# Performance work log

Measured on AMD Instinct MI355X. Metric: run time of the kernel, lower is better.

Reference implementation:

```python
import jax, jax.numpy as jnp
import numpy as np

B, S, D = 4, 2048, 256
H = 8
KD = D  # keras MHA key_dim = input_shape[-1] -> per-head dim equals D
EPS = 1e-5


def layer_norm(x, gamma, beta):
    mu = jnp.mean(x, axis=-1, keepdims=True)
    var = jnp.var(x, axis=-1, keepdims=True)
    return (x - mu) * jax.lax.rsqrt(var + EPS) * gamma + beta


def setup_inputs() -> dict:
    key = jax.random.key(0)
    ks = jax.random.split(key, 12)
    scale = 1.0 / np.sqrt(D)
    inp = {
        "input_query": jax.random.normal(ks[0], (B, S, D), jnp.float32),
        "key": jax.random.normal(ks[1], (B, S, D), jnp.float32),
        "value": jax.random.normal(ks[2], (B, S, D), jnp.float32),
        # LayerNorm params (3 separate norms)
        "gq": jnp.ones((D,), jnp.float32), "bq_ln": jnp.zeros((D,), jnp.float32),
        "gk": jnp.ones((D,), jnp.float32), "bk_ln": jnp.zeros((D,), jnp.float32),
        "gv": jnp.ones((D,), jnp.float32), "bv_ln": jnp.zeros((D,), jnp.float32),
        # MHA projection weights: [D, H, KD] for q/k/v, [H, KD, D] for output
        "Wq": jax.random.normal(ks[3], (D, H, KD), jnp.float32) * scale,
        "bq": jnp.zeros((H, KD), jnp.float32),
        "Wk": jax.random.normal(ks[4], (D, H, KD), jnp.float32) * scale,
        "bk": jnp.zeros((H, KD), jnp.float32),
        "Wv": jax.random.normal(ks[5], (D, H, KD), jnp.float32) * scale,
        "bv": jnp.zeros((H, KD), jnp.float32),
        "Wo": jax.random.normal(ks[6], (H, KD, D), jnp.float32) * scale,
        "bo": jnp.zeros((D,), jnp.float32),
    }
    return inp


def reference(input_query, key, value, gq, bq_ln, gk, bk_ln, gv, bv_ln,
              Wq, bq, Wk, bk, Wv, bv, Wo, bo):
    # pre-LN on each stream
    q_in = layer_norm(input_query, gq, bq_ln)
    k_in = layer_norm(key, gk, bk_ln)
    v_in = layer_norm(value, gv, bv_ln)

    # projections -> [B, S, H, KD]
    q = jnp.einsum('bsd,dhk->bshk', q_in, Wq) + bq
    k = jnp.einsum('bsd,dhk->bshk', k_in, Wk) + bk
    v = jnp.einsum('bsd,dhk->bshk', v_in, Wv) + bv

    # scaled dot-product attention (keras scales query by 1/sqrt(key_dim))
    q = q * (1.0 / np.sqrt(KD)).astype(np.float32)
    scores = jnp.einsum('bqhk,bshk->bhqs', q, k)  # [B, H, Sq, Sk]
    probs = jax.nn.softmax(scores, axis=-1)
    # dropout = 0.0 (inference)
    attn = jnp.einsum('bhqs,bshk->bqhk', probs, v)
    out = jnp.einsum('bqhk,hkd->bqd', attn, Wo) + bo

    return input_query + out
```

## Files before the change

### kernel.cpp

```cpp
#include <hip/hip_runtime.h>

using bf16x8 = __attribute__((ext_vector_type(8))) __bf16;
using f32x4  = __attribute__((ext_vector_type(4))) float;
using f32x16 = __attribute__((ext_vector_type(16))) float;
using uint2v = __attribute__((ext_vector_type(2))) unsigned;
typedef unsigned short u16;
typedef const __attribute__((address_space(1))) void* gas_p;
typedef __attribute__((address_space(3))) void* las_p;

#define LOG2E 1.4426950408889634f

__device__ __forceinline__ u16 f2bf(float f) {
  union { float f; unsigned u; } v; v.f = f;
  unsigned r = v.u + 0x7fffu + ((v.u >> 16) & 1u);
  return (u16)(r >> 16);
}

__device__ __forceinline__ unsigned pkbf(float a, float b) {
  unsigned r;
  asm("v_cvt_pk_bf16_f32 %0, %1, %2" : "=v"(r) : "v"(a), "v"(b));
  return r;
}

__device__ __forceinline__ float exp2v(float x) {
  float r;
  asm("v_exp_f32 %0, %1" : "=v"(r) : "v"(x));
  return r;
}

__device__ __forceinline__ unsigned pk_fp8x4(float a, float b, float c, float d) {
  int w = __builtin_amdgcn_cvt_pk_fp8_f32(a, b, 0, false);
  w = __builtin_amdgcn_cvt_pk_fp8_f32(c, d, w, true);
  return (unsigned)w;
}

__device__ __forceinline__ uint2v swap32(unsigned a, unsigned b) {
  return __builtin_amdgcn_permlane32_swap(a, b, false, false);
}

__device__ __forceinline__ void gload16(const void* g, void* l) {
  __builtin_amdgcn_global_load_lds((gas_p)g, (las_p)l, 16, 0, 0);
}

#define MFMA(a, b, c)   __builtin_amdgcn_mfma_f32_16x16x32_bf16((a), (b), (c), 0, 0, 0)
#define MFMA32(a, b, c) __builtin_amdgcn_mfma_f32_32x32x16_bf16((a), (b), (c), 0, 0, 0)
#define MFMA8(a, b, c)  __builtin_amdgcn_mfma_f32_32x32x16_fp8_fp8((a), (b), (c), 0, 0, 0)

__global__ __launch_bounds__(256) void transpose_conv(
    const float* __restrict__ Wq, const float* __restrict__ Wk,
    const float* __restrict__ Wv, const float* __restrict__ Wo,
    u16* __restrict__ wqt, u16* __restrict__ wkt,
    u16* __restrict__ wvt, u16* __restrict__ wot)
{
  int z = blockIdx.y;
  const float* src = (z == 0) ? Wq : (z == 1) ? Wk : (z == 2) ? Wv : Wo;
  u16* dst = (z == 0) ? wqt : (z == 1) ? wkt : (z == 2) ? wvt : wot;
  int C = (z < 3) ? 2048 : 256;
  int R = (z < 3) ? 256 : 2048;
  int TC = C >> 5;
  int tc = blockIdx.x % TC, tr = blockIdx.x / TC;
  __shared__ float tile[32][33];
  int j = threadIdx.x & 31, i0 = threadIdx.x >> 5;
#pragma unroll
  for (int p = 0; p < 4; p++)
    tile[i0 + p * 8][j] = src[(tr * 32 + i0 + p * 8) * C + tc * 32 + j];
  __syncthreads();
#pragma unroll
  for (int p = 0; p < 4; p++)
    dst[(tc * 32 + i0 + p * 8) * R + tr * 32 + j] = f2bf(tile[j][i0 + p * 8]);
}

__global__ __launch_bounds__(256) void ln3_kernel(
    const float* __restrict__ xq, const float* __restrict__ xk, const float* __restrict__ xv,
    const float* __restrict__ gq, const float* __restrict__ bq,
    const float* __restrict__ gk, const float* __restrict__ bk,
    const float* __restrict__ gv, const float* __restrict__ bv,
    u16* __restrict__ oq, u16* __restrict__ ok, u16* __restrict__ ov)
{
  int z = blockIdx.y;
  const float* x = (z == 0) ? xq : (z == 1) ? xk : xv;
  const float* g = (z == 0) ? gq : (z == 1) ? gk : gv;
  const float* be = (z == 0) ? bq : (z == 1) ? bk : bv;
  u16* o = (z == 0) ? oq : (z == 1) ? ok : ov;
  int w = threadIdx.x >> 6, l = threadIdx.x & 63;
  int row = blockIdx.x * 4 + w;
  float4 x4 = *(const float4*)(x + row * 256 + l * 4);
  float s = x4.x + x4.y + x4.z + x4.w;
  float sq = x4.x * x4.x + x4.y * x4.y + x4.z * x4.z + x4.w * x4.w;
#pragma unroll
  for (int mm = 1; mm < 64; mm <<= 1) { s += __shfl_xor(s, mm); sq += __shfl_xor(sq, mm); }
  float mu = s * (1.f / 256.f);
  float var = sq * (1.f / 256.f) - mu * mu;
  float rs = rsqrtf(var + 1e-5f);
  float4 g4 = *(const float4*)(g + l * 4);
  float4 b4 = *(const float4*)(be + l * 4);
  ushort4 o4;
  o4.x = f2bf((x4.x - mu) * rs * g4.x + b4.x);
  o4.y = f2bf((x4.y - mu) * rs * g4.y + b4.y);
  o4.z = f2bf((x4.z - mu) * rs * g4.z + b4.z);
  o4.w = f2bf((x4.w - mu) * rs * g4.w + b4.w);
  *(ushort4*)(o + row * 256 + l * 4) = o4;
}

__global__ __launch_bounds__(256) void proj_gemm_qk(
    const u16* __restrict__ qn, const u16* __restrict__ kn,
    const u16* __restrict__ wqt, const u16* __restrict__ wkt,
    const float* __restrict__ bq, const float* __restrict__ bk,
    u16* __restrict__ qo, u16* __restrict__ ko)
{
  __shared__ u16 As[128 * 64];
  __shared__ u16 Bs[128 * 64];
  int z = blockIdx.z;
  const u16* A  = z ? kn : qn;
  const u16* Bt = z ? wkt : wqt;
  const float* bias = z ? bk : bq;
  u16* Co = z ? ko : qo;
  float scale = z ? 1.0f : 0.0625f * LOG2E;

  int i0 = blockIdx.x * 128, n0 = blockIdx.y * 128;
  int tid = threadIdx.x, w = tid >> 6, l = tid & 63;
  int wr = w >> 1, wc = w & 1, l15 = l & 15, qv = l >> 4;

  f32x4 acc[4][4] = {};

  for (int k0 = 0; k0 < 256; k0 += 64) {
    __syncthreads();
#pragma unroll
    for (int j = 0; j < 4; j++) {
      int c = (w * 4 + j) * 64 + l;
      int row = c >> 3, co = (c & 7) * 8;
      gload16(A + (i0 + row) * 256 + k0 + co, (char*)As + (w * 4 + j) * 1024);
      gload16(Bt + (n0 + row) * 256 + k0 + co, (char*)Bs + (w * 4 + j) * 1024);
    }
    __syncthreads();
#pragma unroll
    for (int kk = 0; kk < 2; kk++) {
      bf16x8 a[4], bfr[4];
#pragma unroll
      for (int m = 0; m < 4; m++)
        a[m] = *(const bf16x8*)(As + (wr * 64 + m * 16 + l15) * 64 + kk * 32 + qv * 8);
#pragma unroll
      for (int n = 0; n < 4; n++)
        bfr[n] = *(const bf16x8*)(Bs + (wc * 64 + n * 16 + l15) * 64 + kk * 32 + qv * 8);
#pragma unroll
      for (int m = 0; m < 4; m++)
#pragma unroll
        for (int n = 0; n < 4; n++) acc[m][n] = MFMA(bfr[n], a[m], acc[m][n]);
    }
  }

#pragma unroll
  for (int m = 0; m < 4; m++) {
    int row = i0 + wr * 64 + m * 16 + l15;
    int bb = row >> 11, ss = row & 2047;
#pragma unroll
    for (int n = 0; n < 4; n++) {
      int col0 = n0 + wc * 64 + n * 16 + qv * 4;
      float4 bc4 = *(const float4*)(bias + col0);
      int hd = col0 >> 8, kd0 = col0 & 255;
      ushort4 o4;
      o4.x = f2bf((acc[m][n][0] + bc4.x) * scale);
      o4.y = f2bf((acc[m][n][1] + bc4.y) * scale);
      o4.z = f2bf((acc[m][n][2] + bc4.z) * scale);
      o4.w = f2bf((acc[m][n][3] + bc4.w) * scale);
      *(ushort4*)(Co + ((size_t)(bb * 8 + hd) * 2048 + ss) * 256 + kd0) = o4;
    }
  }
}

__global__ __launch_bounds__(256) void proj_gemm_v(
    const u16* __restrict__ vn, const u16* __restrict__ wvt,
    const float* __restrict__ bv, unsigned char* __restrict__ vo)
{
  __shared__ u16 As[128 * 64];
  __shared__ u16 Bs[128 * 64];
  int i0 = blockIdx.x * 128, n0 = blockIdx.y * 128;
  int tid = threadIdx.x, w = tid >> 6, l = tid & 63;
  int wr = w >> 1, wc = w & 1, l15 = l & 15, qv = l >> 4;

  f32x4 acc[4][4] = {};

  for (int k0 = 0; k0 < 256; k0 += 64) {
    __syncthreads();
#pragma unroll
    for (int j = 0; j < 4; j++) {
      int c = (w * 4 + j) * 64 + l;
      int row = c >> 3, co = (c & 7) * 8;
      gload16(vn + (i0 + row) * 256 + k0 + co, (char*)As + (w * 4 + j) * 1024);
      gload16(wvt + (n0 + row) * 256 + k0 + co, (char*)Bs + (w * 4 + j) * 1024);
    }
    __syncthreads();
#pragma unroll
    for (int kk = 0; kk < 2; kk++) {
      bf16x8 a[4], bfr[4];
#pragma unroll
      for (int m = 0; m < 4; m++)
        a[m] = *(const bf16x8*)(As + (wr * 64 + m * 16 + l15) * 64 + kk * 32 + qv * 8);
#pragma unroll
      for (int n = 0; n < 4; n++)
        bfr[n] = *(const bf16x8*)(Bs + (wc * 64 + n * 16 + l15) * 64 + kk * 32 + qv * 8);
#pragma unroll
      for (int m = 0; m < 4; m++)
#pragma unroll
        for (int n = 0; n < 4; n++) acc[m][n] = MFMA(a[m], bfr[n], acc[m][n]);
    }
  }

#pragma unroll
  for (int n = 0; n < 4; n++) {
    int col = n0 + wc * 64 + n * 16 + l15;
    float bc = bv[col];
    int hd = col >> 8, kd = col & 255;
#pragma unroll
    for (int m = 0; m < 4; m++) {
      int row0 = i0 + wr * 64 + m * 16 + qv * 4;
      int bb = row0 >> 11, ss = row0 & 2047;
      unsigned wv = pk_fp8x4(acc[m][n][0] + bc, acc[m][n][1] + bc,
                             acc[m][n][2] + bc, acc[m][n][3] + bc);
      int pos = (ss & ~63) | (((ss >> 3) & 3) << 4) | (((ss >> 5) & 1) << 3) | (ss & 7);
      *(unsigned*)(vo + ((size_t)(bb * 8 + hd) * 256 + kd) * 2048 + pos) = wv;
    }
  }
}

__global__ __launch_bounds__(512, 2) void flash_attn(
    const u16* __restrict__ q, const u16* __restrict__ k,
    const unsigned char* __restrict__ vt, u16* __restrict__ o)
{
  __shared__ char lds[98304];
  int f = blockIdx.x;
  int qt = f >> 5;
  int bh = (f & 7) | (((f >> 3) & 3) << 3);
  int b = bh >> 3, hh = bh & 7;
  int tid = threadIdx.x, w = tid >> 6, l = tid & 63;
  int l31 = l & 31, h = l >> 5;

  const u16* Q = q + (size_t)(bh * 2048 + qt * 256 + w * 32) * 256;
  const u16* K = k + (size_t)bh * 2048 * 256;
  const unsigned char* V = vt + (size_t)bh * 256 * 2048;

  bf16x8 qf[16];
#pragma unroll
  for (int dt = 0; dt < 16; dt++)
    qf[dt] = *(const bf16x8*)(Q + l31 * 256 + dt * 16 + h * 8);

  f32x16 oacc[8] = {};
  float m_ = -1e30f, lsum = 0.f;

  auto stage = [&](int t, char* base) {
#pragma unroll
    for (int j = 0; j < 4; j++) {
      int c = w * 4 + j;
      int off = c * 1024 + l * 16;
      int r = off >> 9, ps = l & 31;
      gload16(K + (size_t)(t * 64 + r) * 256 + ((ps ^ (r & 31)) << 3), base + off);
    }
#pragma unroll
    for (int j = 0; j < 2; j++) {
      int c = w * 2 + j;
      int off = c * 1024 + l * 16;
      int r = off >> 8, pg = (off >> 4) & 15;
      int g = pg ^ (r & 15);
      int d = r + 64 * (g >> 2), sc = g & 3;
      gload16(V + (size_t)d * 2048 + t * 64 + sc * 16, base + 32768 + off);
    }
  };

  stage(0, lds);
  __syncthreads();

  for (int t = 0; t < 32; t++) {
    char* cur = lds + (size_t)(t & 1) * 49152;
    char* nxt = lds + (size_t)((t + 1) & 1) * 49152;
    if (t + 1 < 32) stage(t + 1, nxt);

    f32x16 p0 = {}, p1 = {};
    __builtin_amdgcn_s_setprio(1);
#pragma unroll
    for (int dt = 0; dt < 16; dt++) {
      int sl = ((dt * 2 + h) ^ l31) << 4;
      bf16x8 kf0 = *(const bf16x8*)(cur + l31 * 512 + sl);
      bf16x8 kf1 = *(const bf16x8*)(cur + (32 + l31) * 512 + sl);
      p0 = MFMA32(kf0, qf[dt], p0);
      p1 = MFMA32(kf1, qf[dt], p1);
    }
    __builtin_amdgcn_s_setprio(0);

    float n0 = fmaxf(fmaxf(p0[0], p0[1]), fmaxf(p0[2], p0[3]));
    float n1 = fmaxf(fmaxf(p0[4], p0[5]), fmaxf(p0[6], p0[7]));
    float n2 = fmaxf(fmaxf(p0[8], p0[9]), fmaxf(p0[10], p0[11]));
    float n3 = fmaxf(fmaxf(p0[12], p0[13]), fmaxf(p0[14], p0[15]));
    float n4 = fmaxf(fmaxf(p1[0], p1[1]), fmaxf(p1[2], p1[3]));
    float n5 = fmaxf(fmaxf(p1[4], p1[5]), fmaxf(p1[6], p1[7]));
    float n6 = fmaxf(fmaxf(p1[8], p1[9]), fmaxf(p1[10], p1[11]));
    float n7 = fmaxf(fmaxf(p1[12], p1[13]), fmaxf(p1[14], p1[15]));
    float mt = fmaxf(fmaxf(fmaxf(n0, n1), fmaxf(n2, n3)),
                     fmaxf(fmaxf(n4, n5), fmaxf(n6, n7)));
    {
      uint2v mr = swap32(__builtin_bit_cast(unsigned, mt), __builtin_bit_cast(unsigned, mt));
      mt = fmaxf(__builtin_bit_cast(float, mr.x), __builtin_bit_cast(float, mr.y));
    }
    if (__any(mt > m_ + 7.0f)) {
      float mn = fmaxf(m_, mt);
      float fsc = exp2v(m_ - mn);
      lsum *= fsc;
#pragma unroll
      for (int dt = 0; dt < 8; dt++)
#pragma unroll
        for (int i = 0; i < 16; i++) oacc[dt][i] *= fsc;
      m_ = mn;
    }
#pragma unroll
    for (int i = 0; i < 16; i++) { p0[i] = exp2v(p0[i] - m_); lsum += p0[i]; }
#pragma unroll
    for (int i = 0; i < 16; i++) { p1[i] = exp2v(p1[i] - m_); lsum += p1[i]; }

    unsigned pwf0[4], pwf1[4];
#pragma unroll
    for (int j = 0; j < 4; j++) {
      pwf0[j] = pk_fp8x4(p0[4 * j], p0[4 * j + 1], p0[4 * j + 2], p0[4 * j + 3]);
      pwf1[j] = pk_fp8x4(p1[4 * j], p1[4 * j + 1], p1[4 * j + 2], p1[4 * j + 3]);
    }

#pragma unroll
    for (int k2 = 0; k2 < 2; k2++) {
      uint2v f0 = swap32(pwf0[k2 * 2], pwf0[k2 * 2 + 1]);
      uint2v f1 = swap32(pwf1[k2 * 2], pwf1[k2 * 2 + 1]);
      long long pA = (long long)(((unsigned long long)f0.y << 32) | f0.x);
      long long pB = (long long)(((unsigned long long)f1.y << 32) | f1.x);
      __builtin_amdgcn_s_setprio(1);
#pragma unroll
      for (int dt = 0; dt < 8; dt++) {
        int r = (dt & 1) * 32 + l31;
        int g = (dt >> 1) * 4 + k2 * 2 + h;
        const uint4 vv = *(const uint4*)(cur + 32768 + r * 256 + ((g ^ (r & 15)) << 4));
        long long vA = (long long)(((unsigned long long)vv.y << 32) | vv.x);
        long long vB = (long long)(((unsigned long long)vv.w << 32) | vv.z);
        oacc[dt] = MFMA8(vA, pA, oacc[dt]);
        oacc[dt] = MFMA8(vB, pB, oacc[dt]);
      }
      __builtin_amdgcn_s_setprio(0);
    }

    asm volatile("s_waitcnt vmcnt(0)" ::: "memory");
    __syncthreads();
  }

  __syncthreads();
  float lsc;
  {
    uint2v lr = swap32(__builtin_bit_cast(unsigned, lsum), __builtin_bit_cast(unsigned, lsum));
    lsc = __builtin_bit_cast(float, lr.x) + __builtin_bit_cast(float, lr.y);
  }
  float inv = 1.0f / lsc;
  char* wbase = (char*)lds + w * 8192;
  int qr15 = l31 & 15;
#pragma unroll
  for (int ph = 0; ph < 2; ph++) {
    if ((l31 >> 4) == ph) {
#pragma unroll
      for (int dt = 0; dt < 8; dt++) {
#pragma unroll
        for (int rg = 0; rg < 4; rg++) {
          uint2 uu;
          uu.x = pkbf(oacc[dt][rg * 4 + 0] * inv, oacc[dt][rg * 4 + 1] * inv);
          uu.y = pkbf(oacc[dt][rg * 4 + 2] * inv, oacc[dt][rg * 4 + 3] * inv);
          *(uint2*)(wbase + qr15 * 512 + ((dt * 64 + rg * 16) ^ (qr15 << 4)) + h * 8) = uu;
        }
      }
    }
    asm volatile("s_waitcnt lgkmcnt(0)" ::: "memory");
    __builtin_amdgcn_sched_barrier(0);
#pragma unroll
    for (int c = 0; c < 8; c++) {
      int qr = c * 2 + h;
      uint4 vv = *(const uint4*)(wbase + qr * 512 + ((l31 ^ qr) << 4));
      int s = qt * 256 + w * 32 + ph * 16 + qr;
      *(uint4*)((char*)o + (size_t)(b * 2048 + s) * 4096 + hh * 512 + l31 * 16) = vv;
    }
    asm volatile("s_waitcnt lgkmcnt(0)" ::: "memory");
  }
}

__global__ __launch_bounds__(256) void out_gemm(
    const u16* __restrict__ A, const u16* __restrict__ Bt,
    const float* __restrict__ bo, const float* __restrict__ resid,
    float* __restrict__ out)
{
  __shared__ u16 As[64 * 64];
  __shared__ u16 Bs[64 * 64];
  int i0 = blockIdx.x * 64, n0 = blockIdx.y * 64;
  int tid = threadIdx.x, w = tid >> 6, l = tid & 63, l15 = l & 15, qv = l >> 4;

  f32x4 acc[4] = {};

  for (int k0 = 0; k0 < 2048; k0 += 64) {
    __syncthreads();
#pragma unroll
    for (int j = 0; j < 2; j++) {
      int c = w * 2 + j;
      int off = c * 1024 + l * 16;
      int r = off >> 7, co = (off & 127) >> 1;
      gload16(A + (size_t)(i0 + r) * 2048 + k0 + co, (char*)As + off);
      gload16(Bt + (size_t)(n0 + r) * 2048 + k0 + co, (char*)Bs + off);
    }
    __syncthreads();
#pragma unroll
    for (int kk = 0; kk < 2; kk++) {
      bf16x8 a = *(const bf16x8*)(As + (w * 16 + l15) * 64 + kk * 32 + qv * 8);
      bf16x8 bfr[4];
#pragma unroll
      for (int n = 0; n < 4; n++)
        bfr[n] = *(const bf16x8*)(Bs + (n * 16 + l15) * 64 + kk * 32 + qv * 8);
#pragma unroll
      for (int n = 0; n < 4; n++) acc[n] = MFMA(bfr[n], a, acc[n]);
    }
  }

  int row = i0 + w * 16 + l15;
#pragma unroll
  for (int n = 0; n < 4; n++) {
    int col0 = n0 + n * 16 + qv * 4;
    float4 bc4 = *(const float4*)(bo + col0);
    float4 rs4 = *(const float4*)(resid + (size_t)row * 256 + col0);
    float4 o4;
    o4.x = acc[n][0] + bc4.x + rs4.x;
    o4.y = acc[n][1] + bc4.y + rs4.y;
    o4.z = acc[n][2] + bc4.z + rs4.z;
    o4.w = acc[n][3] + bc4.w + rs4.w;
    *(float4*)(out + (size_t)row * 256 + col0) = o4;
  }
}

extern "C" void kernel_launch(void* const* d_in, const int* in_sizes, int n_in,
                              void* d_out, int out_size, void* d_ws, size_t ws_size,
                              hipStream_t stream)
{
  const float* inq  = (const float*)d_in[0];
  const float* key  = (const float*)d_in[1];
  const float* val  = (const float*)d_in[2];
  const float* gq   = (const float*)d_in[3];
  const float* bqln = (const float*)d_in[4];
  const float* gk   = (const float*)d_in[5];
  const float* bkln = (const float*)d_in[6];
  const float* gv   = (const float*)d_in[7];
  const float* bvln = (const float*)d_in[8];
  const float* Wq   = (const float*)d_in[9];
  const float* bq   = (const float*)d_in[10];
  const float* Wk   = (const float*)d_in[11];
  const float* bk   = (const float*)d_in[12];
  const float* Wv   = (const float*)d_in[13];
  const float* bv   = (const float*)d_in[14];
  const float* Wo   = (const float*)d_in[15];
  const float* bo   = (const float*)d_in[16];

  char* ws = (char*)d_ws;
  const size_t MB = 1ull << 20;
  u16* wqt = (u16*)(ws + 0 * MB);
  u16* wkt = (u16*)(ws + 1 * MB);
  u16* wvt = (u16*)(ws + 2 * MB);
  u16* wot = (u16*)(ws + 3 * MB);
  u16* qn  = (u16*)(ws + 4 * MB);
  u16* kn  = (u16*)(ws + 8 * MB);
  u16* vn  = (u16*)(ws + 12 * MB);
  u16* qws = (u16*)(ws + 16 * MB);
  u16* kws = (u16*)(ws + 48 * MB);
  u16* attn = (u16*)(ws + 80 * MB);
  unsigned char* vtw = (unsigned char*)(ws + 112 * MB);

  transpose_conv<<<dim3(512, 4), 256, 0, stream>>>(Wq, Wk, Wv, Wo, wqt, wkt, wvt, wot);
  ln3_kernel<<<dim3(2048, 3), 256, 0, stream>>>(inq, key, val, gq, bqln, gk, bkln, gv, bvln,
                                                qn, kn, vn);
  proj_gemm_qk<<<dim3(64, 16, 2), 256, 0, stream>>>(qn, kn, wqt, wkt, bq, bk, qws, kws);
  proj_gemm_v<<<dim3(64, 16), 256, 0, stream>>>(vn, wvt, bv, vtw);
  flash_attn<<<256, 512, 0, stream>>>(qws, kws, vtw, attn);
  out_gemm<<<dim3(128, 4), 256, 0, stream>>>(attn, wot, bo, inq, (float*)d_out);
}
```

Baseline: 253.1 us.

## Shrink flash-attn blocks to 4 waves and split K/V staging pipeline

The attention kernel now launches 512 blocks of 256 threads, each covering 128 query rows instead of 256, and changes the block-to-(batch,head) mapping. K tiles stay double-buffered, but V is single-buffered and loaded at the start of each iteration. A partial vmcnt wait plus a barrier sits before the PV stage, so the V load overlaps the QK^T and softmax work. The aim is more blocks for load balance across CUs and a smaller LDS footprint. The cost is that each block reloads all of K and V, doubling K/V traffic, and each iteration has an extra barrier.

```diff
diff --git a/kernel.cpp b/kernel.cpp
--- a/kernel.cpp
+++ b/kernel.cpp
@@ -223,19 +223,20 @@
   }
 }
 
-__global__ __launch_bounds__(512, 2) void flash_attn(
+__global__ __launch_bounds__(256, 2) void flash_attn(
     const u16* __restrict__ q, const u16* __restrict__ k,
     const unsigned char* __restrict__ vt, u16* __restrict__ o)
 {
-  __shared__ char lds[98304];
+  __shared__ char lds[81920];
   int f = blockIdx.x;
-  int qt = f >> 5;
-  int bh = (f & 7) | (((f >> 3) & 3) << 3);
+  int idx = f >> 3;
+  int bh = (f & 7) * 4 + (idx & 3);
+  int qt = idx >> 2;
   int b = bh >> 3, hh = bh & 7;
   int tid = threadIdx.x, w = tid >> 6, l = tid & 63;
   int l31 = l & 31, h = l >> 5;
 
-  const u16* Q = q + (size_t)(bh * 2048 + qt * 256 + w * 32) * 256;
+  const u16* Q = q + (size_t)(bh * 2048 + qt * 128 + w * 32) * 256;
   const u16* K = k + (size_t)bh * 2048 * 256;
   const unsigned char* V = vt + (size_t)bh * 256 * 2048;
 
@@ -247,40 +248,45 @@
   f32x16 oacc[8] = {};
   float m_ = -1e30f, lsum = 0.f;
 
-  auto stage = [&](int t, char* base) {
-#pragma unroll
-    for (int j = 0; j < 4; j++) {
-      int c = w * 4 + j;
+  auto stageK = [&](int t, int slot) {
+    char* base = lds + (size_t)slot * 32768;
+#pragma unroll
+    for (int j = 0; j < 8; j++) {
+      int c = w * 8 + j;
       int off = c * 1024 + l * 16;
       int r = off >> 9, ps = l & 31;
       gload16(K + (size_t)(t * 64 + r) * 256 + ((ps ^ (r & 31)) << 3), base + off);
     }
-#pragma unroll
-    for (int j = 0; j < 2; j++) {
-      int c = w * 2 + j;
+  };
+  auto stageV = [&](int t) {
+    char* base = lds + 65536;
+#pragma unroll
+    for (int j = 0; j < 4; j++) {
+      int c = w * 4 + j;
       int off = c * 1024 + l * 16;
       int r = off >> 8, pg = (off >> 4) & 15;
       int g = pg ^ (r & 15);
       int d = r + 64 * (g >> 2), sc = g & 3;
-      gload16(V + (size_t)d * 2048 + t * 64 + sc * 16, base + 32768 + off);
+      gload16(V + (size_t)d * 2048 + t * 64 + sc * 16, base + off);
     }
   };
 
-  stage(0, lds);
+  stageK(0, 0);
+  asm volatile("s_waitcnt vmcnt(0)" ::: "memory");
   __syncthreads();
 
   for (int t = 0; t < 32; t++) {
-    char* cur = lds + (size_t)(t & 1) * 49152;
-    char* nxt = lds + (size_t)((t + 1) & 1) * 49152;
-    if (t + 1 < 32) stage(t + 1, nxt);
+    const char* kb = lds + (size_t)(t & 1) * 32768;
+    stageV(t);
+    if (t + 1 < 32) stageK(t + 1, (t + 1) & 1);
 
     f32x16 p0 = {}, p1 = {};
     __builtin_amdgcn_s_setprio(1);
 #pragma unroll
     for (int dt = 0; dt < 16; dt++) {
       int sl = ((dt * 2 + h) ^ l31) << 4;
-      bf16x8 kf0 = *(const bf16x8*)(cur + l31 * 512 + sl);
-      bf16x8 kf1 = *(const bf16x8*)(cur + (32 + l31) * 512 + sl);
+      bf16x8 kf0 = *(const bf16x8*)(kb + l31 * 512 + sl);
+      bf16x8 kf1 = *(const bf16x8*)(kb + (32 + l31) * 512 + sl);
       p0 = MFMA32(kf0, qf[dt], p0);
       p1 = MFMA32(kf1, qf[dt], p1);
     }
@@ -322,6 +328,15 @@
       pwf1[j] = pk_fp8x4(p1[4 * j], p1[4 * j + 1], p1[4 * j + 2], p1[4 * j + 3]);
     }
 
+    if (t + 1 < 32) {
+      asm volatile("s_waitcnt vmcnt(8)" ::: "memory");
+    } else {
+      asm volatile("s_waitcnt vmcnt(0)" ::: "memory");
+    }
+    __builtin_amdgcn_sched_barrier(0);
+    __builtin_amdgcn_s_barrier();
+
+    const char* vb = lds + 65536;
 #pragma unroll
     for (int k2 = 0; k2 < 2; k2++) {
       uint2v f0 = swap32(pwf0[k2 * 2], pwf0[k2 * 2 + 1]);
@@ -333,7 +348,7 @@
       for (int dt = 0; dt < 8; dt++) {
         int r = (dt & 1) * 32 + l31;
         int g = (dt >> 1) * 4 + k2 * 2 + h;
-        const uint4 vv = *(const uint4*)(cur + 32768 + r * 256 + ((g ^ (r & 15)) << 4));
+        const uint4 vv = *(const uint4*)(vb + r * 256 + ((g ^ (r & 15)) << 4));
         long long vA = (long long)(((unsigned long long)vv.y << 32) | vv.x);
         long long vB = (long long)(((unsigned long long)vv.w << 32) | vv.z);
         oacc[dt] = MFMA8(vA, pA, oacc[dt]);
@@ -343,7 +358,8 @@
     }
 
     asm volatile("s_waitcnt vmcnt(0)" ::: "memory");
-    __syncthreads();
+    __builtin_amdgcn_sched_barrier(0);
+    __builtin_amdgcn_s_barrier();
   }
 
   __syncthreads();
@@ -375,7 +391,7 @@
     for (int c = 0; c < 8; c++) {
       int qr = c * 2 + h;
       uint4 vv = *(const uint4*)(wbase + qr * 512 + ((l31 ^ qr) << 4));
-      int s = qt * 256 + w * 32 + ph * 16 + qr;
+      int s = qt * 128 + w * 32 + ph * 16 + qr;
       *(uint4*)((char*)o + (size_t)(b * 2048 + s) * 4096 + hh * 512 + l31 * 16) = vv;
     }
     asm volatile("s_waitcnt lgkmcnt(0)" ::: "memory");
@@ -473,6 +489,6 @@
                                                 qn, kn, vn);
   proj_gemm_qk<<<dim3(64, 16, 2), 256, 0, stream>>>(qn, kn, wqt, wkt, bq, bk, qws, kws);
   proj_gemm_v<<<dim3(64, 16), 256, 0, stream>>>(vn, wvt, bv, vtw);
-  flash_attn<<<256, 512, 0, stream>>>(qws, kws, vtw, attn);
+  flash_attn<<<512, 256, 0, stream>>>(qws, kws, vtw, attn);
   out_gemm<<<dim3(128, 4), 256, 0, stream>>>(attn, wot, bo, inq, (float*)d_out);
 }
```

Measured after the change: 304.6 us. 1.2x slower.
